# Kernel optimization log

Hardware: AMD Instinct MI355X
Metric: run time of the kernel (lower is better)

The kernel has to match this reference:

```python
import jax, jax.numpy as jnp
import numpy as np


def setup_inputs() -> dict:
    key = jax.random.key(0)
    k1, k2 = jax.random.split(key)
    center = jax.random.normal(k1, (4096,), dtype=jnp.float32)
    error = jax.random.normal(k2, (8192, 4096), dtype=jnp.float32) * 0.01
    return {"center": center, "error": error}


def reference(center, error):
    # Zonotope ReLU abstract transformer.
    center_orig_shape = center.shape
    error_orig_shape = error.shape
    c = center.reshape(-1)                      # (d,)
    e = error.reshape(error.shape[0], -1)       # (n_error, d)
    n_error, d = e.shape

    apt = jnp.sum(jnp.abs(e), axis=0)           # (d,) interval radius
    ub = c + apt
    lb = c - apt

    cross = (ub > 0) & (lb < 0)                 # unstable neurons
    act = lb >= 0                               # stably active
    # dead (ub <= 0): slope = 0, mu = 0 -> center/error zeroed

    denom = jnp.where(cross, ub - lb, jnp.float32(1.0))
    slope = jnp.where(cross, ub / denom, jnp.float32(0.0))
    mu = jnp.where(cross, -slope * lb * jnp.float32(0.5), jnp.float32(0.0))

    new_center = jnp.where(act, c, slope * c + mu)          # (d,)
    col_scale = jnp.where(act, jnp.float32(1.0), slope)     # (d,)
    top = e * col_scale[None, :]                             # (n_error, d)
    # One fresh error term per crossing neuron; padded to d rows (diagonal),
    # zero rows where the neuron is not crossing (static output shape).
    bottom = jnp.diag(mu)                                    # (d, d)
    new_error = jnp.concatenate([top, bottom], axis=0)       # (n_error + d, d)

    new_center = new_center.reshape(center_orig_shape)
    new_error = new_error.reshape((n_error + d,) + error_orig_shape[1:])
    return new_center, new_error
```

## Files before the change

kernel.cpp:

```cpp
#include <hip/hip_runtime.h>

#define D      4096
#define NERR   8192
#define DF4    (D / 4)
#define NBLK   256
#define NSTRIP 128
#define HROWS  (NERR / 2)
#define TPB    1024
#define RPP    (TPB / 8)
#define NPASS  (HROWS / RPP)
#define NWAVE  (TPB / 64)

typedef float f32x4 __attribute__((ext_vector_type(4)));

__global__ __launch_bounds__(TPB) void k_reduce(const f32x4* __restrict__ e4,
                                                f32x4* __restrict__ part4) {
    __shared__ f32x4 wred[NWAVE * 8];

    const int t    = threadIdx.x;
    const int lane = t & 63;
    const int w    = t >> 6;
    const int cf   = t & 7;
    const int r0   = t >> 3;
    const int s    = blockIdx.x >> 1;
    const int h    = blockIdx.x & 1;
    const int off  = s * 8 + cf;
    const size_t rbase = (size_t)h * HROWS;

    f32x4 acc = (f32x4)(0.f, 0.f, 0.f, 0.f);
    #pragma unroll 8
    for (int k = 0; k < NPASS; ++k) {
        f32x4 v = e4[(rbase + k * RPP + r0) * DF4 + off];
        acc.x += fabsf(v.x);
        acc.y += fabsf(v.y);
        acc.z += fabsf(v.z);
        acc.w += fabsf(v.w);
    }
    #pragma unroll
    for (int st = 8; st <= 32; st <<= 1) {
        acc.x += __shfl_xor(acc.x, st, 64);
        acc.y += __shfl_xor(acc.y, st, 64);
        acc.z += __shfl_xor(acc.z, st, 64);
        acc.w += __shfl_xor(acc.w, st, 64);
    }
    if (lane < 8) wred[w * 8 + lane] = acc;
    __syncthreads();

    if (t < 8) {
        f32x4 sum = wred[t];
        #pragma unroll
        for (int w2 = 1; w2 < NWAVE; ++w2) sum += wred[w2 * 8 + t];
        part4[(size_t)(s * 2 + h) * 8 + t] = sum;
    }
}

__global__ __launch_bounds__(TPB) void k_emit(const f32x4* __restrict__ e4,
                                              const f32x4* __restrict__ part4,
                                              const f32x4* __restrict__ c4,
                                              f32x4* __restrict__ oc4,
                                              f32x4* __restrict__ top4,
                                              f32x4* __restrict__ bot4) {
    __shared__ f32x4 scl[8];
    __shared__ f32x4 muL[8];

    const int t    = threadIdx.x;
    const int cf   = t & 7;
    const int r0   = t >> 3;
    const int s    = blockIdx.x >> 1;
    const int h    = blockIdx.x & 1;
    const int off  = s * 8 + cf;
    const size_t rbase = (size_t)h * HROWS;

    if (t < 8) {
        const int g = s * 8 + t;
        const f32x4 apt = part4[(size_t)(s * 2) * 8 + t]
                        + part4[(size_t)(s * 2 + 1) * 8 + t];
        const f32x4 cen = c4[g];
        f32x4 oc, cs, mu4;
        #pragma unroll
        for (int j = 0; j < 4; ++j) {
            const float c  = cen[j];
            const float ub = c + apt[j];
            const float lb = c - apt[j];
            const bool cross = (ub > 0.f) && (lb < 0.f);
            const bool act   = (lb >= 0.f);
            const float denom = cross ? (ub - lb) : 1.f;
            const float slope = cross ? (ub / denom) : 0.f;
            const float mu    = cross ? (-slope * lb * 0.5f) : 0.f;
            oc[j]  = act ? c : (slope * c + mu);
            cs[j]  = act ? 1.f : slope;
            mu4[j] = mu;
        }
        scl[t] = cs;
        muL[t] = mu4;
        if (h == 0) oc4[g] = oc;
    }
    __syncthreads();

    const f32x4 cs = scl[cf];
    #pragma unroll 8
    for (int k = 0; k < NPASS; ++k) {
        const size_t idx = (rbase + k * RPP + r0) * DF4 + off;
        f32x4 v = e4[idx];
        v *= cs;
        __builtin_nontemporal_store(v, &top4[idx]);
    }

    const int w    = t >> 6;
    const int lane = t & 63;
    const int r    = 32 * s + 16 * h + w;
    const int dg   = r >> 2;
    const float muv = muL[(r >> 2) - 8 * s][r & 3];
    #pragma unroll
    for (int j = 0; j < 16; ++j) {
        const int c = lane + j * 64;
        f32x4 v = (f32x4)(0.f, 0.f, 0.f, 0.f);
        if (c == dg) v[r & 3] = muv;
        __builtin_nontemporal_store(v, &bot4[(size_t)r * DF4 + c]);
    }
}

extern "C" void kernel_launch(void* const* d_in, const int* in_sizes, int n_in,
                              void* d_out, int out_size, void* d_ws, size_t ws_size,
                              hipStream_t stream) {
    const float* center = (const float*)d_in[0];
    const float* error  = (const float*)d_in[1];
    float* out = (float*)d_out;

    float* out_center = out;
    float* out_top    = out + D;
    float* out_bottom = out + (size_t)D + (size_t)NERR * D;

    f32x4* part4 = (f32x4*)d_ws;

    k_reduce<<<NBLK, TPB, 0, stream>>>(
        (const f32x4*)error, part4);
    k_emit<<<NBLK, TPB, 0, stream>>>(
        (const f32x4*)error, part4, (const f32x4*)center,
        (f32x4*)out_center, (f32x4*)out_top, (f32x4*)out_bottom);
}
```

Baseline: 72.01 us.

## Fuse reduce and emit kernels with pairwise inter-block spin barrier

Merges the column-abs-sum kernel and the scaling/emit kernel into one launch. Each pair of blocks sharing a column strip exchanges partial sums through global memory and an atomic counter barrier, then proceeds to scale and write outputs. This removes one kernel launch and lets the second read of the error strip likely hit in cache. The cost is an added memset, and the barrier relies on both blocks of a pair being co-resident; with 256 blocks of 1024 threads this is plausible but not guaranteed.

```diff
diff --git a/kernel.cpp b/kernel.cpp
--- a/kernel.cpp
+++ b/kernel.cpp
@@ -3,19 +3,26 @@
 #define D      4096
 #define NERR   8192
 #define DF4    (D / 4)
-#define NBLK   256
-#define NSTRIP 128
 #define HROWS  (NERR / 2)
 #define TPB    1024
 #define RPP    (TPB / 8)
 #define NPASS  (HROWS / RPP)
 #define NWAVE  (TPB / 64)
+#define NBLK   256
 
 typedef float f32x4 __attribute__((ext_vector_type(4)));
 
-__global__ __launch_bounds__(TPB) void k_reduce(const f32x4* __restrict__ e4,
-                                                f32x4* __restrict__ part4) {
+__global__ __launch_bounds__(TPB) void k_fused(const f32x4* __restrict__ e4,
+                                               const f32x4* __restrict__ c4,
+                                               f32x4* __restrict__ oc4,
+                                               f32x4* __restrict__ top4,
+                                               f32x4* __restrict__ bot4,
+                                               float* __restrict__ partf,
+                                               int*   __restrict__ bar) {
     __shared__ f32x4 wred[NWAVE * 8];
+    __shared__ float aptL[32];
+    __shared__ f32x4 scl[8];
+    __shared__ f32x4 muL[8];
 
     const int t    = threadIdx.x;
     const int lane = t & 63;
@@ -46,42 +53,42 @@
     if (lane < 8) wred[w * 8 + lane] = acc;
     __syncthreads();
 
-    if (t < 8) {
-        f32x4 sum = wred[t];
+    if (t < 32) {
+        const int f4 = t >> 2, cm = t & 3;
+        float sum = 0.f;
         #pragma unroll
-        for (int w2 = 1; w2 < NWAVE; ++w2) sum += wred[w2 * 8 + t];
-        part4[(size_t)(s * 2 + h) * 8 + t] = sum;
+        for (int w2 = 0; w2 < NWAVE; ++w2) sum += wred[w2 * 8 + f4][cm];
+        __hip_atomic_store(&partf[(2 * s + h) * 32 + t], sum,
+                           __ATOMIC_RELAXED, __HIP_MEMORY_SCOPE_AGENT);
     }
-}
+    __syncthreads();
 
-__global__ __launch_bounds__(TPB) void k_emit(const f32x4* __restrict__ e4,
-                                              const f32x4* __restrict__ part4,
-                                              const f32x4* __restrict__ c4,
-                                              f32x4* __restrict__ oc4,
-                                              f32x4* __restrict__ top4,
-                                              f32x4* __restrict__ bot4) {
-    __shared__ f32x4 scl[8];
-    __shared__ f32x4 muL[8];
+    if (t == 0) {
+        __threadfence();
+        __hip_atomic_fetch_add(&bar[s], 1, __ATOMIC_RELEASE,
+                               __HIP_MEMORY_SCOPE_AGENT);
+        while (__hip_atomic_load(&bar[s], __ATOMIC_ACQUIRE,
+                                 __HIP_MEMORY_SCOPE_AGENT) < 2) {}
+    }
+    __syncthreads();
 
-    const int t    = threadIdx.x;
-    const int cf   = t & 7;
-    const int r0   = t >> 3;
-    const int s    = blockIdx.x >> 1;
-    const int h    = blockIdx.x & 1;
-    const int off  = s * 8 + cf;
-    const size_t rbase = (size_t)h * HROWS;
+    if (t < 32)
+        aptL[t] = __hip_atomic_load(&partf[(2 * s) * 32 + t],
+                                    __ATOMIC_RELAXED, __HIP_MEMORY_SCOPE_AGENT)
+                + __hip_atomic_load(&partf[(2 * s + 1) * 32 + t],
+                                    __ATOMIC_RELAXED, __HIP_MEMORY_SCOPE_AGENT);
+    __syncthreads();
 
     if (t < 8) {
         const int g = s * 8 + t;
-        const f32x4 apt = part4[(size_t)(s * 2) * 8 + t]
-                        + part4[(size_t)(s * 2 + 1) * 8 + t];
         const f32x4 cen = c4[g];
         f32x4 oc, cs, mu4;
         #pragma unroll
         for (int j = 0; j < 4; ++j) {
+            const float apt = aptL[t * 4 + j];
             const float c  = cen[j];
-            const float ub = c + apt[j];
-            const float lb = c - apt[j];
+            const float ub = c + apt;
+            const float lb = c - apt;
             const bool cross = (ub > 0.f) && (lb < 0.f);
             const bool act   = (lb >= 0.f);
             const float denom = cross ? (ub - lb) : 1.f;
@@ -106,10 +113,8 @@
         __builtin_nontemporal_store(v, &top4[idx]);
     }
 
-    const int w    = t >> 6;
-    const int lane = t & 63;
-    const int r    = 32 * s + 16 * h + w;
-    const int dg   = r >> 2;
+    const int r  = 32 * s + 16 * h + w;
+    const int dg = r >> 2;
     const float muv = muL[(r >> 2) - 8 * s][r & 3];
     #pragma unroll
     for (int j = 0; j < 16; ++j) {
@@ -126,16 +131,19 @@
     const float* center = (const float*)d_in[0];
     const float* error  = (const float*)d_in[1];
     float* out = (float*)d_out;
+    float* ws  = (float*)d_ws;
+
+    float* partf = ws;
+    int*   bar   = (int*)(ws + 256 * 32);
 
     float* out_center = out;
     float* out_top    = out + D;
     float* out_bottom = out + (size_t)D + (size_t)NERR * D;
 
-    f32x4* part4 = (f32x4*)d_ws;
+    hipMemsetAsync(bar, 0, 128 * sizeof(int), stream);
 
-    k_reduce<<<NBLK, TPB, 0, stream>>>(
-        (const f32x4*)error, part4);
-    k_emit<<<NBLK, TPB, 0, stream>>>(
-        (const f32x4*)error, part4, (const f32x4*)center,
-        (f32x4*)out_center, (f32x4*)out_top, (f32x4*)out_bottom);
+    k_fused<<<NBLK, TPB, 0, stream>>>(
+        (const f32x4*)error, (const f32x4*)center,
+        (f32x4*)out_center, (f32x4*)out_top, (f32x4*)out_bottom,
+        partf, bar);
 }
```

After: 88.59 us. 1.23x slower.
